# Kernel tuning notes

Measured on AMD Instinct MI355X. Metric: run time of the kernel, lower is better.

The kernel has to match this reference:

```python
import jax, jax.numpy as jnp
import numpy as np

V, D, L, ITERS, B, S = 30522, 256, 4, 10, 256, 512
UPDATE_RATE = 0.1


def _lin(x, w, b):
    # torch nn.Linear: y = x @ W^T + b, w: [out, in]
    return jnp.matmul(x, w.T) + b


def setup_inputs() -> dict:
    key = jax.random.key(0)
    ks = jax.random.split(key, 20)
    s = 0.02
    inp = {
        "input_ids": jax.random.randint(ks[0], (B, S), 0, V),
        "embedding": jax.random.normal(ks[1], (V, D), jnp.float32) * s,
        "pos_enc": jax.random.normal(ks[2], (1, S, D), jnp.float32) * s,
        # stacked per-layer PredictiveCodingLayer params [L, ...]
        "init_w": jax.random.normal(ks[3], (L, D, D), jnp.float32) * s,
        "init_b": jnp.zeros((L, D), jnp.float32),
        "pred_w": jax.random.normal(ks[4], (L, D, D), jnp.float32) * s,
        "pred_b": jnp.zeros((L, D), jnp.float32),
        "upd_w": jax.random.normal(ks[5], (L, D, D), jnp.float32) * s,
        "upd_b": jnp.zeros((L, D), jnp.float32),
        "start_q_w": jax.random.normal(ks[6], (D, D), jnp.float32) * s,
        "start_q_b": jnp.zeros((D,), jnp.float32),
        "end_q_w": jax.random.normal(ks[7], (D, D), jnp.float32) * s,
        "end_q_b": jnp.zeros((D,), jnp.float32),
        "key_w": jax.random.normal(ks[8], (D, D), jnp.float32) * s,
        "key_b": jnp.zeros((D,), jnp.float32),
        "ans_w1": jax.random.normal(ks[9], (D // 2, D), jnp.float32) * s,
        "ans_b1": jnp.zeros((D // 2,), jnp.float32),
        "ans_w2": jax.random.normal(ks[10], (2, D // 2), jnp.float32) * s,
        "ans_b2": jnp.zeros((2,), jnp.float32),
    }
    return inp


def reference(input_ids, embedding, pos_enc, init_w, init_b, pred_w, pred_b,
              upd_w, upd_b, start_q_w, start_q_b, end_q_w, end_q_b,
              key_w, key_b, ans_w1, ans_b1, ans_w2, ans_b2):
    seq_len = input_ids.shape[1]
    embeds = embedding[input_ids] + pos_enc[:, :seq_len, :]   # [B,S,D]
    pooled = jnp.mean(embeds, axis=1)                          # [B,D]

    predict = lambda i, r: _lin(r, pred_w[i], pred_b[i])

    # init_representation: tanh(Linear(x)) chained across layers
    reps = []
    cur = pooled
    for i in range(L):
        cur = jnp.tanh(_lin(cur, init_w[i], init_b[i]))
        reps.append(cur)
    ff_output = reps[-1]

    # iterative predictive-coding refinement
    for _ in range(ITERS):
        errors = [pooled - predict(0, reps[0])]
        for i in range(1, L):
            errors.append(jax.lax.stop_gradient(reps[i - 1]) - predict(i, reps[i]))
        new_reps = []
        for i in range(L):
            if i < L - 1:  # bidirectional
                error_above = reps[i] - predict(i + 1, reps[i + 1])
            else:
                error_above = jnp.zeros_like(reps[i])
            total_error = errors[i] + 0.5 * error_above
            # update: rep + rate * tanh(Linear(error))
            new_reps.append(reps[i] + UPDATE_RATE * jnp.tanh(_lin(total_error, upd_w[i], upd_b[i])))
        reps = new_reps

    refined = reps[-1] + ff_output                             # [B,D]
    token_keys = _lin(embeds, key_w, key_b)                    # [B,S,D]
    start_q = _lin(refined, start_q_w, start_q_b)
    end_q = _lin(refined, end_q_w, end_q_b)
    start_logits = jnp.einsum('bd,bsd->bs', start_q, token_keys)
    end_logits = jnp.einsum('bd,bsd->bs', end_q, token_keys)
    h = jax.nn.gelu(_lin(refined, ans_w1, ans_b1), approximate=False)
    answerable_logits = _lin(h, ans_w2, ans_b2)                # [B,2]
    return (start_logits, end_logits, answerable_logits)
```

## Files before the change

kernel.cpp:

```cpp
#include <hip/hip_runtime.h>
#include <math.h>

#define NB 256
#define NS 512
#define ND 256
#define NL 4
#define NITERS 10
#define DD (ND*ND)

__global__ __launch_bounds__(256) void k_pool1(const int* __restrict__ ids,
                                               const float* __restrict__ emb,
                                               const float* __restrict__ pos,
                                               float* __restrict__ partial) {
    const int bid = blockIdx.x;
    const int b = bid >> 2, q = bid & 3;
    const int t = threadIdx.x;
    __shared__ int sid[128];
    if (t < 128) sid[t] = ids[b * NS + q * 128 + t];
    __syncthreads();
    float acc = 0.f;
#pragma unroll 8
    for (int s = 0; s < 128; ++s)
        acc += emb[(size_t)sid[s] * ND + t] + pos[(q * 128 + s) * ND + t];
    partial[bid * ND + t] = acc;
}

__global__ __launch_bounds__(256) void k_prep(
    const float* __restrict__ pred_w, const float* __restrict__ pred_b,
    const float* __restrict__ upd_w,  const float* __restrict__ upd_b,
    const float* __restrict__ init_w,
    const float* __restrict__ sw, const float* __restrict__ sb,
    const float* __restrict__ ew, const float* __restrict__ eb,
    const float* __restrict__ kw, const float* __restrict__ kb,
    const float* __restrict__ w1,
    const float* __restrict__ partial,
    float* __restrict__ CM, float* __restrict__ CMI,
    float* __restrict__ KSt, float* __restrict__ KEt, float* __restrict__ W1t,
    float* __restrict__ cvec, float* __restrict__ rc0,
    float* __restrict__ vsk, float* __restrict__ vse,
    float* __restrict__ ksb, float* __restrict__ keb, float* __restrict__ scal)
{
    const int bid = blockIdx.x;
    const int t = threadIdx.x;

    if (bid < 576 || (bid >= 1056 && bid < 1120)) {
        int id, tile;
        if (bid < 576) { id = bid >> 6; tile = bid & 63; }
        else           { id = 9;        tile = bid - 1056; }
        const float* Asrc = nullptr; const float* Bsrc = nullptr;
        float alpha = 1.f, tau = 0.f; float* outp = nullptr;
        bool bT = false, aPool = false;
        switch (id) {
            case 0: Asrc = pred_w;        Bsrc = upd_w;        alpha=-1.f;  tau=0.5f; outp = CM + 0*(size_t)DD; break;
            case 1: Asrc = pred_w + DD;   Bsrc = upd_w;        alpha=-0.5f;           outp = CM + 1*(size_t)DD; break;
            case 2: Asrc = pred_w + DD;   Bsrc = upd_w + DD;   alpha=-1.f;  tau=0.5f; outp = CM + 4*(size_t)DD; break;
            case 3: Asrc = pred_w + 2*DD; Bsrc = upd_w + DD;   alpha=-0.5f;           outp = CM + 5*(size_t)DD; break;
            case 4: Asrc = pred_w + 2*DD; Bsrc = upd_w + 2*DD; alpha=-1.f;  tau=0.5f; outp = CM + 7*(size_t)DD; break;
            case 5: Asrc = pred_w + 3*DD; Bsrc = upd_w + 2*DD; alpha=-0.5f;           outp = CM + 8*(size_t)DD; break;
            case 6: Asrc = pred_w + 3*DD; Bsrc = upd_w + 3*DD; alpha=-1.f;            outp = CM + 10*(size_t)DD; break;
            case 7: Asrc = sw; Bsrc = kw; bT = true; outp = KSt; break;
            case 8: Asrc = ew; Bsrc = kw; bT = true; outp = KEt; break;
            default: Bsrc = upd_w; aPool = true; outp = rc0; break;
        }
        const float* Tsrc = (tau != 0.f) ? Bsrc : nullptr;
        const int i0 = (tile >> 3) * 32, j0 = (tile & 7) * 32;
        __shared__ float As[32 * 33];
        __shared__ float Bs[32 * 33];
        const int tx = t & 15, ty = t >> 4;
        float a00 = 0.f, a01 = 0.f, a10 = 0.f, a11 = 0.f;
        for (int e0 = 0; e0 < 256; e0 += 32) {
            __syncthreads();
            if (!aPool) {
                const int ii = t & 31, e8 = t >> 5;
#pragma unroll
                for (int p = 0; p < 4; ++p) {
                    int ee = e8 + 8 * p;
                    As[ee * 33 + ii] = Asrc[(size_t)(e0 + ee) * 256 + i0 + ii];
                }
            } else {
                const int ee = t & 31, i8 = t >> 5;
#pragma unroll
                for (int p = 0; p < 4; ++p) {
                    int ii = i8 + 8 * p;
                    const float* pp = partial + (size_t)(i0 + ii) * 4 * 256 + e0 + ee;
                    As[ee * 33 + ii] = (pp[0] + pp[256] + pp[512] + pp[768]) * (1.f / 512.f);
                }
            }
            if (!bT) {
                const int ee = t & 31, j8 = t >> 5;
#pragma unroll
                for (int p = 0; p < 4; ++p) {
                    int jj = j8 + 8 * p;
                    Bs[ee * 33 + jj] = Bsrc[(size_t)(j0 + jj) * 256 + e0 + ee];
                }
            } else {
                const int jj = t & 31, e8 = t >> 5;
#pragma unroll
                for (int p = 0; p < 4; ++p) {
                    int ee = e8 + 8 * p;
                    Bs[ee * 33 + jj] = Bsrc[(size_t)(e0 + ee) * 256 + j0 + jj];
                }
            }
            __syncthreads();
#pragma unroll
            for (int e = 0; e < 32; ++e) {
                float va0 = As[e * 33 + 2 * ty], va1 = As[e * 33 + 2 * ty + 1];
                float vb0 = Bs[e * 33 + 2 * tx], vb1 = Bs[e * 33 + 2 * tx + 1];
                a00 += va0 * vb0; a01 += va0 * vb1;
                a10 += va1 * vb0; a11 += va1 * vb1;
            }
        }
        float t00 = 0.f, t01 = 0.f, t10 = 0.f, t11 = 0.f;
        if (Tsrc) {
            t00 = Tsrc[(size_t)(j0 + 2 * tx) * 256 + i0 + 2 * ty];
            t01 = Tsrc[(size_t)(j0 + 2 * tx + 1) * 256 + i0 + 2 * ty];
            t10 = Tsrc[(size_t)(j0 + 2 * tx) * 256 + i0 + 2 * ty + 1];
            t11 = Tsrc[(size_t)(j0 + 2 * tx + 1) * 256 + i0 + 2 * ty + 1];
        }
        outp[(size_t)(i0 + 2 * ty) * 256 + j0 + 2 * tx]         = alpha * a00 + tau * t00;
        outp[(size_t)(i0 + 2 * ty) * 256 + j0 + 2 * tx + 1]     = alpha * a01 + tau * t01;
        outp[(size_t)(i0 + 2 * ty + 1) * 256 + j0 + 2 * tx]     = alpha * a10 + tau * t10;
        outp[(size_t)(i0 + 2 * ty + 1) * 256 + j0 + 2 * tx + 1] = alpha * a11 + tau * t11;
        return;
    }

    if (bid < 1024) {
        const int tid = bid - 576;
        const int m = tid >> 6, tile = tid & 63;
        const float* src; float* dst;
        if (m < 3) { src = upd_w + (size_t)(m + 1) * DD; dst = CM + (size_t)(3 + 3 * m) * DD; }
        else       { src = init_w + (size_t)(m - 3) * DD; dst = CMI + (size_t)(m - 3) * DD; }
        const int r0 = (tile >> 3) * 32, c0 = (tile & 7) * 32;
        __shared__ float T[32 * 33];
        const int cc = t & 31, r8 = t >> 5;
#pragma unroll
        for (int p = 0; p < 4; ++p) {
            int rr = r8 + 8 * p;
            T[rr * 33 + cc] = src[(size_t)(r0 + rr) * 256 + c0 + cc];
        }
        __syncthreads();
#pragma unroll
        for (int p = 0; p < 4; ++p) {
            int rr = r8 + 8 * p;
            dst[(size_t)(c0 + rr) * 256 + r0 + cc] = T[cc * 33 + rr];
        }
        return;
    }

    if (bid < 1056) {
        const int tile = bid - 1024;
        const int e0 = (tile >> 2) * 32, j0 = (tile & 3) * 32;
        __shared__ float T[32 * 33];
        const int cc = t & 31, r8 = t >> 5;
#pragma unroll
        for (int p = 0; p < 4; ++p) {
            int jj = r8 + 8 * p;
            T[jj * 33 + cc] = w1[(size_t)(j0 + jj) * 256 + e0 + cc];
        }
        __syncthreads();
#pragma unroll
        for (int p = 0; p < 4; ++p) {
            int ee = r8 + 8 * p;
            W1t[(size_t)(e0 + ee) * 128 + j0 + cc] = T[cc * 33 + ee];
        }
        return;
    }

    const int vb = bid - 1120;
    if (vb < 4) {
        const int l = vb;
        __shared__ float v[256];
        v[t] = (l < 3) ? pred_b[l * 256 + t] + 0.5f * pred_b[(l + 1) * 256 + t]
                       : pred_b[3 * 256 + t];
        __syncthreads();
        const float* U = upd_w + (size_t)l * DD + (size_t)t * 256;
        float acc = 0.f;
#pragma unroll 8
        for (int k = 0; k < 256; k += 4) {
            float4 u = *(const float4*)&U[k];
            acc += u.x * v[k] + u.y * v[k + 1] + u.z * v[k + 2] + u.w * v[k + 3];
        }
        cvec[l * 256 + t] = upd_b[l * 256 + t] - acc;
        return;
    }
    {
        const float* W = (vb == 4) ? sw : ew;
        const float* bb = (vb == 4) ? sb : eb;
        float* vout = (vb == 4) ? vsk : vse;
        float* bout = (vb == 4) ? ksb : keb;
        __shared__ float kbv[256], bbv[256], red[256];
        kbv[t] = kb[t]; bbv[t] = bb[t];
        __syncthreads();
        float a1 = 0.f, a2 = 0.f;
#pragma unroll 4
        for (int k = 0; k < 256; ++k) {
            a1 += W[(size_t)k * 256 + t] * kbv[k];
            a2 += kw[(size_t)k * 256 + t] * bbv[k];
        }
        vout[t] = a1; bout[t] = a2;
        red[t] = kbv[t] * bbv[t];
        __syncthreads();
        for (int s = 128; s > 0; s >>= 1) {
            if (t < s) red[t] += red[t + s];
            __syncthreads();
        }
        if (t == 0) scal[vb - 4] = red[0];
        return;
    }
}

__global__ __launch_bounds__(256) void k_init(const float* __restrict__ partial,
                                              const float* __restrict__ CMI,
                                              const float* __restrict__ init_b,
                                              float* __restrict__ rA,
                                              float* __restrict__ ff)
{
    const int row = blockIdx.x, t = threadIdx.x;
    __shared__ float xs[256];
    {
        const float* p = partial + (size_t)row * 4 * 256 + t;
        xs[t] = (p[0] + p[256] + p[512] + p[768]) * (1.f / 512.f);
    }
    float* rrow = rA + (size_t)row * 1024;
    for (int il = 0; il < 4; ++il) {
        __syncthreads();
        const float* M = CMI + (size_t)il * DD + t;
        float a0 = 0.f, a1 = 0.f, a2 = 0.f, a3 = 0.f;
#pragma unroll 8
        for (int k = 0; k < 256; k += 4) {
            float4 xv = *(const float4*)&xs[k];
            a0 += M[(size_t)(k + 0) * 256] * xv.x;
            a1 += M[(size_t)(k + 1) * 256] * xv.y;
            a2 += M[(size_t)(k + 2) * 256] * xv.z;
            a3 += M[(size_t)(k + 3) * 256] * xv.w;
        }
        float vx = tanhf(a0 + a1 + a2 + a3 + init_b[il * 256 + t]);
        __syncthreads();
        xs[t] = vx;
        rrow[il * 256 + t] = vx;
        if (il == 3) ff[(size_t)row * 256 + t] = vx;
    }
}

__global__ __launch_bounds__(512, 2) void k_stage(const float* __restrict__ rcur,
                                                  const float* __restrict__ CM,
                                                  const float* __restrict__ cvec,
                                                  const float* __restrict__ rc0,
                                                  float* __restrict__ rnxt)
{
    __shared__ float As[32 * 136];
    __shared__ float Bs[32 * 136];
    __shared__ float4 scr[128 * 17];
    const int bid = blockIdx.x;
    const int t = threadIdx.x;
    const int rowtile = bid >> 5, cg = bid & 31;
    const int l = cg >> 3, dbase = (cg & 7) * 32;
    const int slo = (l == 0) ? 0 : (l - 1);
    const int nj = (l == 0 || l == 3) ? 2 : 3;
    const int KK = nj * 256;
    const int nch = KK >> 7;
    const int r0 = rowtile * 32;
    const int slotBase = l * 3;

    const int pos = t & 15, s = t >> 4;
    const int pr = pos >> 2, pc = pos & 3;
    const int r0t = pr * 8, c0t = pc * 8;
    const int keyA = pr << 2, keyB = pc << 2;
    const int sa_r = t >> 4, sa_f = t & 15;
    const int sb_k = t >> 2, sb_d = t & 3;

    float acc[8][8];
#pragma unroll
    for (int i = 0; i < 8; ++i)
#pragma unroll
        for (int j = 0; j < 8; ++j) acc[i][j] = 0.f;

    const float* aSrc = rcur + (size_t)(r0 + sa_r) * 1024 + slo * 256;
    float4 pa0 = *(const float4*)&aSrc[sa_f * 4];
    float4 pa1 = *(const float4*)&aSrc[sa_f * 4 + 64];
    float4 qb0, qb1;
    {
        const float* bp = CM + (size_t)slotBase * DD + (size_t)sb_k * 256 + dbase + sb_d * 8;
        qb0 = *(const float4*)&bp[0];
        qb1 = *(const float4*)&bp[4];
    }

    const int aw0 = sa_r * 136 + 4 * (sa_f ^ ((sa_r >> 3) << 2));
    const int aw1 = sa_r * 136 + 4 * ((sa_f + 16) ^ ((sa_r >> 3) << 2));
    const int kswz = 4 * ((sb_k >> 2) ^ (sb_d << 2)) + (sb_k & 3);
    const int bw0 = (sb_d * 8) * 136 + kswz;

    for (int c = 0; c < nch; ++c) {
        *(float4*)&As[aw0] = pa0;
        *(float4*)&As[aw1] = pa1;
        Bs[bw0 + 0 * 136] = qb0.x; Bs[bw0 + 1 * 136] = qb0.y;
        Bs[bw0 + 2 * 136] = qb0.z; Bs[bw0 + 3 * 136] = qb0.w;
        Bs[bw0 + 4 * 136] = qb1.x; Bs[bw0 + 5 * 136] = qb1.y;
        Bs[bw0 + 6 * 136] = qb1.z; Bs[bw0 + 7 * 136] = qb1.w;
        __syncthreads();
        if (c + 1 < nch) {
            const int kg = (c + 1) * 128;
            pa0 = *(const float4*)&aSrc[kg + sa_f * 4];
            pa1 = *(const float4*)&aSrc[kg + sa_f * 4 + 64];
            const float* bp = CM + (size_t)(slotBase + (kg >> 8)) * DD
                            + (size_t)((kg & 255) + sb_k) * 256 + dbase + sb_d * 8;
            qb0 = *(const float4*)&bp[0];
            qb1 = *(const float4*)&bp[4];
        }
        float4 ar[8], bc[8];
        const int ka = 4 * (s ^ keyA), kb = 4 * (s ^ keyB);
#pragma unroll
        for (int rr = 0; rr < 8; ++rr)
            ar[rr] = *(const float4*)&As[(r0t + rr) * 136 + ka];
#pragma unroll
        for (int cc = 0; cc < 8; ++cc)
            bc[cc] = *(const float4*)&Bs[(c0t + cc) * 136 + kb];
#pragma unroll
        for (int rr = 0; rr < 8; ++rr)
#pragma unroll
            for (int cc = 0; cc < 8; ++cc)
                acc[rr][cc] += ar[rr].x * bc[cc].x + ar[rr].y * bc[cc].y
                             + ar[rr].z * bc[cc].z + ar[rr].w * bc[cc].w;
        __syncthreads();
    }

#pragma unroll
    for (int rr = 0; rr < 8; ++rr)
#pragma unroll
        for (int cc = 0; cc < 8; ++cc) {
            float v = acc[rr][cc];
            v += __shfl_xor(v, 16);
            v += __shfl_xor(v, 32);
            acc[rr][cc] = v;
        }
    const int wave = t >> 6, lane = t & 63;
    if (lane < 16) {
#pragma unroll
        for (int rr = 0; rr < 8; ++rr) {
            scr[(wave * 16 + lane) * 17 + rr * 2 + 0] =
                make_float4(acc[rr][0], acc[rr][1], acc[rr][2], acc[rr][3]);
            scr[(wave * 16 + lane) * 17 + rr * 2 + 1] =
                make_float4(acc[rr][4], acc[rr][5], acc[rr][6], acc[rr][7]);
        }
    }
    __syncthreads();
    if (t < 256) {
        const int rf = t >> 3, cq = t & 7;
        const int pos2 = (rf >> 3) * 4 + (cq >> 1);
        const int idx = pos2 * 17 + (rf & 7) * 2 + (cq & 1);
        float4 sum = scr[idx];
#pragma unroll
        for (int w = 1; w < 8; ++w) {
            float4 v = scr[w * 16 * 17 + idx];
            sum.x += v.x; sum.y += v.y; sum.z += v.z; sum.w += v.w;
        }
        const int dcol = dbase + cq * 4;
        const int grow = r0 + rf;
        float4 cv = *(const float4*)&cvec[l * 256 + dcol];
        float z0 = sum.x + cv.x, z1 = sum.y + cv.y;
        float z2 = sum.z + cv.z, z3 = sum.w + cv.w;
        if (l == 0) {
            float4 rc = *(const float4*)&rc0[(size_t)grow * 256 + dcol];
            z0 += rc.x; z1 += rc.y; z2 += rc.z; z3 += rc.w;
        }
        float4 rold = *(const float4*)&rcur[(size_t)grow * 1024 + l * 256 + dcol];
        float4 o;
        o.x = rold.x + 0.1f * tanhf(z0);
        o.y = rold.y + 0.1f * tanhf(z1);
        o.z = rold.z + 0.1f * tanhf(z2);
        o.w = rold.w + 0.1f * tanhf(z3);
        *(float4*)&rnxt[(size_t)grow * 1024 + l * 256 + dcol] = o;
    }
}

__global__ __launch_bounds__(256) void k_heads(const float* __restrict__ rA,
    const float* __restrict__ ff,
    const float* __restrict__ KSt, const float* __restrict__ KEt,
    const float* __restrict__ ksb, const float* __restrict__ keb,
    const float* __restrict__ vsk, const float* __restrict__ vse,
    const float* __restrict__ scal,
    const float* __restrict__ W1t, const float* __restrict__ b1,
    const float* __restrict__ w2, const float* __restrict__ b2,
    float* __restrict__ sqk, float* __restrict__ eqk,
    float* __restrict__ sqb, float* __restrict__ eqb,
    float* __restrict__ out)
{
    const int row = blockIdx.x, t = threadIdx.x;
    __shared__ float xs[256];
    __shared__ float red[256];
    __shared__ float hp[256];
    __shared__ float hs[128];
    xs[t] = rA[(size_t)row * 1024 + 768 + t] + ff[(size_t)row * 256 + t];
    __syncthreads();
    {
        float a0 = 0.f, a1 = 0.f, a2 = 0.f, a3 = 0.f;
        float e0 = 0.f, e1 = 0.f, e2 = 0.f, e3 = 0.f;
        const float* KS = KSt + t;
        const float* KE = KEt + t;
#pragma unroll 4
        for (int f = 0; f < 256; f += 4) {
            float4 xv = *(const float4*)&xs[f];
            a0 += KS[(size_t)(f + 0) * 256] * xv.x; a1 += KS[(size_t)(f + 1) * 256] * xv.y;
            a2 += KS[(size_t)(f + 2) * 256] * xv.z; a3 += KS[(size_t)(f + 3) * 256] * xv.w;
            e0 += KE[(size_t)(f + 0) * 256] * xv.x; e1 += KE[(size_t)(f + 1) * 256] * xv.y;
            e2 += KE[(size_t)(f + 2) * 256] * xv.z; e3 += KE[(size_t)(f + 3) * 256] * xv.w;
        }
        sqk[(size_t)row * 256 + t] = a0 + a1 + a2 + a3 + ksb[t];
        eqk[(size_t)row * 256 + t] = e0 + e1 + e2 + e3 + keb[t];
    }
    red[t] = vsk[t] * xs[t];
    __syncthreads();
    for (int s = 128; s > 0; s >>= 1) { if (t < s) red[t] += red[t + s]; __syncthreads(); }
    if (t == 0) sqb[row] = red[0] + scal[0];
    __syncthreads();
    red[t] = vse[t] * xs[t];
    __syncthreads();
    for (int s = 128; s > 0; s >>= 1) { if (t < s) red[t] += red[t + s]; __syncthreads(); }
    if (t == 0) eqb[row] = red[0] + scal[1];
    __syncthreads();
    {
        const int j = t & 127, half = t >> 7;
        float a = 0.f;
        const float* W = W1t + (size_t)half * 128 * 128 + j;
        const float* xh = &xs[half * 128];
#pragma unroll 8
        for (int e = 0; e < 128; ++e) a += W[(size_t)e * 128] * xh[e];
        hp[half * 128 + j] = a;
    }
    __syncthreads();
    if (t < 128) {
        float x = hp[t] + hp[128 + t] + b1[t];
        hs[t] = 0.5f * x * (1.f + erff(x * 0.70710678118654752f));
    }
    __syncthreads();
    if (t < 128) { red[t] = hs[t] * w2[t]; red[128 + t] = hs[t] * w2[128 + t]; }
    __syncthreads();
    for (int s = 64; s > 0; s >>= 1) {
        if (t < s) red[t] += red[t + s];
        else if (t >= 128 && t < 128 + s) red[t] += red[t + s];
        __syncthreads();
    }
    if (t == 0)   out[2 * NB * NS + row * 2 + 0] = red[0] + b2[0];
    if (t == 128) out[2 * NB * NS + row * 2 + 1] = red[128] + b2[1];
}

__global__ __launch_bounds__(512) void k_logits(const int* __restrict__ ids,
                                                const float* __restrict__ emb,
                                                const float* __restrict__ pos,
                                                const float* __restrict__ sqk,
                                                const float* __restrict__ eqk,
                                                const float* __restrict__ sqb,
                                                const float* __restrict__ eqb,
                                                float* __restrict__ out) {
    const int bid = blockIdx.x;
    const int b = bid >> 2, q = bid & 3;
    const int t = threadIdx.x;
    __shared__ float sk[ND], ek[ND];
    __shared__ int sid[128];
    if (t < 256) sk[t] = sqk[b * ND + t];
    else ek[t - 256] = eqk[b * ND + t - 256];
    if (t < 128) sid[t] = ids[b * NS + q * 128 + t];
    __syncthreads();
    const int w = t >> 6, lane = t & 63;
    const float4 ks = *(const float4*)&sk[4 * lane];
    const float4 ke = *(const float4*)&ek[4 * lane];
    const float qbs = sqb[b], qbe = eqb[b];
    for (int si = w; si < 128; si += 8) {
        const int s = q * 128 + si;
        const int id = sid[si];
        const float4 e4 = *(const float4*)&emb[(size_t)id * ND + 4 * lane];
        const float4 p4 = *(const float4*)&pos[s * ND + 4 * lane];
        float vx = e4.x + p4.x, vy = e4.y + p4.y, vz = e4.z + p4.z, vw = e4.w + p4.w;
        float ds = vx * ks.x + vy * ks.y + vz * ks.z + vw * ks.w;
        float de = vx * ke.x + vy * ke.y + vz * ke.z + vw * ke.w;
#pragma unroll
        for (int off = 32; off >= 1; off >>= 1) {
            ds += __shfl_xor(ds, off);
            de += __shfl_xor(de, off);
        }
        if (lane == 0) {
            out[b * NS + s] = ds + qbs;
            out[NB * NS + b * NS + s] = de + qbe;
        }
    }
}

extern "C" void kernel_launch(void* const* d_in, const int* in_sizes, int n_in,
                              void* d_out, int out_size, void* d_ws, size_t ws_size,
                              hipStream_t stream) {
    const int*   ids    = (const int*)d_in[0];
    const float* emb    = (const float*)d_in[1];
    const float* pos    = (const float*)d_in[2];
    const float* init_w = (const float*)d_in[3];
    const float* init_b = (const float*)d_in[4];
    const float* pred_w = (const float*)d_in[5];
    const float* pred_b = (const float*)d_in[6];
    const float* upd_w  = (const float*)d_in[7];
    const float* upd_b  = (const float*)d_in[8];
    const float* sw     = (const float*)d_in[9];
    const float* sb     = (const float*)d_in[10];
    const float* ew     = (const float*)d_in[11];
    const float* eb     = (const float*)d_in[12];
    const float* kw     = (const float*)d_in[13];
    const float* kb     = (const float*)d_in[14];
    const float* w1     = (const float*)d_in[15];
    const float* b1     = (const float*)d_in[16];
    const float* w2     = (const float*)d_in[17];
    const float* b2     = (const float*)d_in[18];
    float* out = (float*)d_out;

    float* ws = (float*)d_ws;
    float* partial = ws;                 ws += 1024 * 256;
    float* rA      = ws;                 ws += 256 * 1024;
    float* rB      = ws;                 ws += 256 * 1024;
    float* ff      = ws;                 ws += 256 * 256;
    float* CM      = ws;                 ws += 12 * DD;
    float* CMI     = ws;                 ws += 4 * DD;
    float* KSt     = ws;                 ws += DD;
    float* KEt     = ws;                 ws += DD;
    float* W1t     = ws;                 ws += 256 * 128;
    float* cvec    = ws;                 ws += 4 * 256;
    float* rc0     = ws;                 ws += 256 * 256;
    float* vsk     = ws;                 ws += 256;
    float* vse     = ws;                 ws += 256;
    float* ksb     = ws;                 ws += 256;
    float* keb     = ws;                 ws += 256;
    float* scal    = ws;                 ws += 8;
    float* sqk     = ws;                 ws += 256 * 256;
    float* eqk     = ws;                 ws += 256 * 256;
    float* sqb     = ws;                 ws += 256;
    float* eqb     = ws;                 ws += 256;

    k_pool1<<<1024, 256, 0, stream>>>(ids, emb, pos, partial);

    k_prep<<<1126, 256, 0, stream>>>(pred_w, pred_b, upd_w, upd_b, init_w,
                                     sw, sb, ew, eb, kw, kb, w1, partial,
                                     CM, CMI, KSt, KEt, W1t,
                                     cvec, rc0, vsk, vse, ksb, keb, scal);

    k_init<<<256, 256, 0, stream>>>(partial, CMI, init_b, rA, ff);

    float* cur = rA;
    float* nxt = rB;
    for (int it = 0; it < NITERS; ++it) {
        k_stage<<<256, 512, 0, stream>>>(cur, CM, cvec, rc0, nxt);
        float* tmp = cur; cur = nxt; nxt = tmp;
    }

    k_heads<<<256, 256, 0, stream>>>(rA, ff, KSt, KEt, ksb, keb, vsk, vse, scal,
                                     W1t, b1, w2, b2, sqk, eqk, sqb, eqb, out);

    k_logits<<<1024, 512, 0, stream>>>(ids, emb, pos, sqk, eqk, sqb, eqb, out);
}
```

Before: 238.1 us.

## Preload full B slice into LDS and give each wave its own A rows

The stage kernel now loads the whole K-by-32 weight slice into shared memory once at block start. Each of 4 waves owns 8 rows of A staged in a private LDS region, so the per-chunk block-wide barriers go away. The K-split reduction changes from cross-wave to within-wave shuffles plus a per-wave LDS scratch, and the block shrinks from 512 to 256 threads. This cuts synchronisation and repeated B staging, at the cost of larger LDS use (about 100KB), which may limit occupancy, and fewer threads per block.

```diff
diff --git a/kernel.cpp b/kernel.cpp
--- a/kernel.cpp
+++ b/kernel.cpp
@@ -7,6 +7,8 @@
 #define NL 4
 #define NITERS 10
 #define DD (ND*ND)
+#define BSTR 780
+#define ASTR 132
 
 __global__ __launch_bounds__(256) void k_pool1(const int* __restrict__ ids,
                                                const float* __restrict__ emb,
@@ -242,15 +244,14 @@
     }
 }
 
-__global__ __launch_bounds__(512, 2) void k_stage(const float* __restrict__ rcur,
-                                                  const float* __restrict__ CM,
-                                                  const float* __restrict__ cvec,
-                                                  const float* __restrict__ rc0,
-                                                  float* __restrict__ rnxt)
+__global__ __launch_bounds__(256) void k_stage(const float* __restrict__ rcur,
+                                               const float* __restrict__ CM,
+                                               const float* __restrict__ cvec,
+                                               const float* __restrict__ rc0,
+                                               float* __restrict__ rnxt)
 {
-    __shared__ float As[32 * 136];
-    __shared__ float Bs[32 * 136];
-    __shared__ float4 scr[128 * 17];
+    __shared__ float Bs[32 * BSTR];
+    __shared__ float As[4 * 8 * ASTR];
     const int bid = blockIdx.x;
     const int t = threadIdx.x;
     const int rowtile = bid >> 5, cg = bid & 31;
@@ -262,12 +263,23 @@
     const int r0 = rowtile * 32;
     const int slotBase = l * 3;
 
-    const int pos = t & 15, s = t >> 4;
-    const int pr = pos >> 2, pc = pos & 3;
-    const int r0t = pr * 8, c0t = pc * 8;
-    const int keyA = pr << 2, keyB = pc << 2;
-    const int sa_r = t >> 4, sa_f = t & 15;
-    const int sb_k = t >> 2, sb_d = t & 3;
+    {
+        const int col4 = (t & 7) * 4, k32 = t >> 3;
+        const float* src = CM + (size_t)slotBase * DD + dbase + col4;
+        for (int k = k32; k < KK; k += 32) {
+            float4 v = *(const float4*)&src[(size_t)k * 256];
+            Bs[(col4 + 0) * BSTR + k] = v.x;
+            Bs[(col4 + 1) * BSTR + k] = v.y;
+            Bs[(col4 + 2) * BSTR + k] = v.z;
+            Bs[(col4 + 3) * BSTR + k] = v.w;
+        }
+    }
+    __syncthreads();
+
+    const int wv = t >> 6, lane = t & 63;
+    const int arow = lane >> 3, af = lane & 7;
+    const int cpair = lane & 3, ks = lane >> 2;
+    float* Aw = As + wv * (8 * ASTR);
 
     float acc[8][8];
 #pragma unroll
@@ -275,53 +287,43 @@
 #pragma unroll
         for (int j = 0; j < 8; ++j) acc[i][j] = 0.f;
 
-    const float* aSrc = rcur + (size_t)(r0 + sa_r) * 1024 + slo * 256;
-    float4 pa0 = *(const float4*)&aSrc[sa_f * 4];
-    float4 pa1 = *(const float4*)&aSrc[sa_f * 4 + 64];
-    float4 qb0, qb1;
-    {
-        const float* bp = CM + (size_t)slotBase * DD + (size_t)sb_k * 256 + dbase + sb_d * 8;
-        qb0 = *(const float4*)&bp[0];
-        qb1 = *(const float4*)&bp[4];
-    }
-
-    const int aw0 = sa_r * 136 + 4 * (sa_f ^ ((sa_r >> 3) << 2));
-    const int aw1 = sa_r * 136 + 4 * ((sa_f + 16) ^ ((sa_r >> 3) << 2));
-    const int kswz = 4 * ((sb_k >> 2) ^ (sb_d << 2)) + (sb_k & 3);
-    const int bw0 = (sb_d * 8) * 136 + kswz;
+    const float* aSrc = rcur + (size_t)(r0 + wv * 8 + arow) * 1024 + slo * 256;
+
+    float4 pa0 = *(const float4*)&aSrc[af * 4];
+    float4 pa1 = *(const float4*)&aSrc[af * 4 + 32];
+    float4 pa2 = *(const float4*)&aSrc[af * 4 + 64];
+    float4 pa3 = *(const float4*)&aSrc[af * 4 + 96];
 
     for (int c = 0; c < nch; ++c) {
-        *(float4*)&As[aw0] = pa0;
-        *(float4*)&As[aw1] = pa1;
-        Bs[bw0 + 0 * 136] = qb0.x; Bs[bw0 + 1 * 136] = qb0.y;
-        Bs[bw0 + 2 * 136] = qb0.z; Bs[bw0 + 3 * 136] = qb0.w;
-        Bs[bw0 + 4 * 136] = qb1.x; Bs[bw0 + 5 * 136] = qb1.y;
-        Bs[bw0 + 6 * 136] = qb1.z; Bs[bw0 + 7 * 136] = qb1.w;
-        __syncthreads();
+        *(float4*)&Aw[arow * ASTR + af * 4]      = pa0;
+        *(float4*)&Aw[arow * ASTR + af * 4 + 32] = pa1;
+        *(float4*)&Aw[arow * ASTR + af * 4 + 64] = pa2;
+        *(float4*)&Aw[arow * ASTR + af * 4 + 96] = pa3;
         if (c + 1 < nch) {
             const int kg = (c + 1) * 128;
-            pa0 = *(const float4*)&aSrc[kg + sa_f * 4];
-            pa1 = *(const float4*)&aSrc[kg + sa_f * 4 + 64];
-            const float* bp = CM + (size_t)(slotBase + (kg >> 8)) * DD
-                            + (size_t)((kg & 255) + sb_k) * 256 + dbase + sb_d * 8;
-            qb0 = *(const float4*)&bp[0];
-            qb1 = *(const float4*)&bp[4];
-        }
-        float4 ar[8], bc[8];
-        const int ka = 4 * (s ^ keyA), kb = 4 * (s ^ keyB);
-#pragma unroll
-        for (int rr = 0; rr < 8; ++rr)
-            ar[rr] = *(const float4*)&As[(r0t + rr) * 136 + ka];
-#pragma unroll
-        for (int cc = 0; cc < 8; ++cc)
-            bc[cc] = *(const float4*)&Bs[(c0t + cc) * 136 + kb];
-#pragma unroll
-        for (int rr = 0; rr < 8; ++rr)
+            pa0 = *(const float4*)&aSrc[kg + af * 4];
+            pa1 = *(const float4*)&aSrc[kg + af * 4 + 32];
+            pa2 = *(const float4*)&aSrc[kg + af * 4 + 64];
+            pa3 = *(const float4*)&aSrc[kg + af * 4 + 96];
+        }
+#pragma unroll
+        for (int h = 0; h < 2; ++h) {
+            float4 ar[8], bc[8];
+            const int ka = h * 64 + ks * 4;
+            const int kb = c * 128 + h * 64 + ks * 4;
+#pragma unroll
+            for (int rr = 0; rr < 8; ++rr)
+                ar[rr] = *(const float4*)&Aw[rr * ASTR + ka];
 #pragma unroll
             for (int cc = 0; cc < 8; ++cc)
-                acc[rr][cc] += ar[rr].x * bc[cc].x + ar[rr].y * bc[cc].y
-                             + ar[rr].z * bc[cc].z + ar[rr].w * bc[cc].w;
-        __syncthreads();
+                bc[cc] = *(const float4*)&Bs[(cpair * 8 + cc) * BSTR + kb];
+#pragma unroll
+            for (int rr = 0; rr < 8; ++rr)
+#pragma unroll
+                for (int cc = 0; cc < 8; ++cc)
+                    acc[rr][cc] += ar[rr].x * bc[cc].x + ar[rr].y * bc[cc].y
+                                 + ar[rr].z * bc[cc].z + ar[rr].w * bc[cc].w;
+        }
     }
 
 #pragma unroll
@@ -329,36 +331,36 @@
 #pragma unroll
         for (int cc = 0; cc < 8; ++cc) {
             float v = acc[rr][cc];
-            v += __shfl_xor(v, 16);
-            v += __shfl_xor(v, 32);
+            v += __shfl_xor(v, 4);
+            v += __shfl_xor(v, 8);
             acc[rr][cc] = v;
         }
-    const int wave = t >> 6, lane = t & 63;
-    if (lane < 16) {
+
+    if ((lane & 12) == 0) {
+        const int ksg = lane >> 4;
+        float* w = Aw + ((ksg * 4 + cpair) << 6);
 #pragma unroll
         for (int rr = 0; rr < 8; ++rr) {
-            scr[(wave * 16 + lane) * 17 + rr * 2 + 0] =
-                make_float4(acc[rr][0], acc[rr][1], acc[rr][2], acc[rr][3]);
-            scr[(wave * 16 + lane) * 17 + rr * 2 + 1] =
-                make_float4(acc[rr][4], acc[rr][5], acc[rr][6], acc[rr][7]);
-        }
-    }
-    __syncthreads();
-    if (t < 256) {
-        const int rf = t >> 3, cq = t & 7;
-        const int pos2 = (rf >> 3) * 4 + (cq >> 1);
-        const int idx = pos2 * 17 + (rf & 7) * 2 + (cq & 1);
-        float4 sum = scr[idx];
-#pragma unroll
-        for (int w = 1; w < 8; ++w) {
-            float4 v = scr[w * 16 * 17 + idx];
-            sum.x += v.x; sum.y += v.y; sum.z += v.z; sum.w += v.w;
-        }
-        const int dcol = dbase + cq * 4;
-        const int grow = r0 + rf;
+            *(float4*)&w[rr * 8]     = make_float4(acc[rr][0], acc[rr][1], acc[rr][2], acc[rr][3]);
+            *(float4*)&w[rr * 8 + 4] = make_float4(acc[rr][4], acc[rr][5], acc[rr][6], acc[rr][7]);
+        }
+    }
+    {
+        const int out_rr = lane >> 3, out_cc4 = (lane >> 2) & 1, out_cp = lane & 3;
+        const int off = out_rr * 8 + out_cc4 * 4;
+        float4 s0 = *(const float4*)&Aw[((0 * 4 + out_cp) << 6) + off];
+        float4 s1 = *(const float4*)&Aw[((1 * 4 + out_cp) << 6) + off];
+        float4 s2 = *(const float4*)&Aw[((2 * 4 + out_cp) << 6) + off];
+        float4 s3 = *(const float4*)&Aw[((3 * 4 + out_cp) << 6) + off];
+        float z0 = s0.x + s1.x + s2.x + s3.x;
+        float z1 = s0.y + s1.y + s2.y + s3.y;
+        float z2 = s0.z + s1.z + s2.z + s3.z;
+        float z3 = s0.w + s1.w + s2.w + s3.w;
+
+        const int grow = r0 + wv * 8 + out_rr;
+        const int dcol = dbase + out_cp * 8 + out_cc4 * 4;
         float4 cv = *(const float4*)&cvec[l * 256 + dcol];
-        float z0 = sum.x + cv.x, z1 = sum.y + cv.y;
-        float z2 = sum.z + cv.z, z3 = sum.w + cv.w;
+        z0 += cv.x; z1 += cv.y; z2 += cv.z; z3 += cv.w;
         if (l == 0) {
             float4 rc = *(const float4*)&rc0[(size_t)grow * 256 + dcol];
             z0 += rc.x; z1 += rc.y; z2 += rc.z; z3 += rc.w;
@@ -543,7 +545,7 @@
     float* cur = rA;
     float* nxt = rB;
     for (int it = 0; it < NITERS; ++it) {
-        k_stage<<<256, 512, 0, stream>>>(cur, CM, cvec, rc0, nxt);
+        k_stage<<<256, 256, 0, stream>>>(cur, CM, cvec, rc0, nxt);
         float* tmp = cur; cur = nxt; nxt = tmp;
     }
 
```

New measurement: 233.0 us. 2.1% less time.
